# Kernel optimization log

Hardware: AMD Instinct MI355X
Metric: run time of the kernel (lower is better)

Reference implementation:

```python
import jax, jax.numpy as jnp
import numpy as np

# Reconstructed GTS forecasting module (DCGRU encoder-decoder, eval mode / no teacher forcing).
N = 5000        # nodes_num
U = 32          # rnn_units
IN = 1          # node_features per step
K = 2           # max_diffusion_step -> supports [X, A@X, A@A@X]
T_ENC = 12
T_DEC = 12
DIN = (K + 1) * (IN + U)


def setup_inputs() -> dict:
    key = jax.random.key(0)
    ks = jax.random.split(key, 12)
    def p(k, shape, scale=0.1):
        return jax.random.normal(k, shape, dtype=jnp.float32) * scale
    inputs = jax.random.normal(ks[0], (N, T_ENC), dtype=jnp.float32)
    targets = jax.random.normal(ks[1], (N, T_DEC), dtype=jnp.float32)
    adj = jax.random.uniform(ks[2], (N, N), dtype=jnp.float32)
    adj = adj / jnp.sum(adj, axis=1, keepdims=True)  # random-walk normalized support
    return {
        'inputs': inputs, 'targets': targets, 'adj_matrix': adj,
        'enc_Wg': p(ks[3], (DIN, 2 * U)), 'enc_bg': jnp.zeros((2 * U,), jnp.float32),
        'enc_Wc': p(ks[4], (DIN, U)),     'enc_bc': jnp.zeros((U,), jnp.float32),
        'dec_Wg': p(ks[5], (DIN, 2 * U)), 'dec_bg': jnp.zeros((2 * U,), jnp.float32),
        'dec_Wc': p(ks[6], (DIN, U)),     'dec_bc': jnp.zeros((U,), jnp.float32),
        'dec_Wp': p(ks[7], (U, 1)),       'dec_bp': jnp.zeros((1,), jnp.float32),
    }


def _gconv(x, h, adj, W, b):
    # diffusion graph convolution over supports [I, A, A^2]
    xh = jnp.concatenate([x, h], axis=-1)          # [N, IN+U]
    x1 = adj @ xh                                  # [N, IN+U]
    x2 = adj @ x1                                  # [N, IN+U]
    return jnp.concatenate([xh, x1, x2], axis=-1) @ W + b


def _dcgru_step(x, h, adj, Wg, bg, Wc, bc):
    ru = jax.nn.sigmoid(_gconv(x, h, adj, Wg, bg))  # [N, 2U]
    r, u = jnp.split(ru, 2, axis=-1)
    c = jnp.tanh(_gconv(x, r * h, adj, Wc, bc))
    return u * h + (1.0 - u) * c


def reference(inputs, targets, adj_matrix, enc_Wg, enc_bg, enc_Wc, enc_bc,
              dec_Wg, dec_bg, dec_Wc, dec_bc, dec_Wp, dec_bp):
    # ---- encoder: scan DCGRU over encoder_length timesteps ----
    def enc_step(h, xt):  # xt: [N]
        h = _dcgru_step(xt[:, None], h, adj_matrix, enc_Wg, enc_bg, enc_Wc, enc_bc)
        return h, None
    h0 = jnp.zeros((N, U), inputs.dtype)
    h_enc, _ = jax.lax.scan(enc_step, h0, inputs.T)
    go = jnp.zeros((N, 1), inputs.dtype)
    def dec_step(carry, _):
        h, x = carry
        h = _dcgru_step(x, h, adj_matrix, dec_Wg, dec_bg, dec_Wc, dec_bc)
        out = h @ dec_Wp + dec_bp  # [N, 1]
        return (h, out), out
    _, outs = jax.lax.scan(dec_step, (h_enc, go), None, length=T_DEC)
    # torch.cat(outputs, dim=-1) -> [N, T_DEC]
    return outs[:, :, 0].T
```

## Files before the change

kernel.cpp:

```cpp
#include <hip/hip_runtime.h>
#include <type_traits>

constexpr int NN = 5000;
constexpr int NP = 5120;
constexpr int TT = 12;
constexpr int UU = 32;
constexpr int FP = 48;
constexpr int FR = 33;
constexpr int DN = 99;
constexpr int BN = 16;
constexpr int KC = 128;
constexpr int NKC = NP / KC;
constexpr int CPW = NKC / 8;
constexpr int GRID_MM = (NN + BN - 1) / BN;
constexpr int CHE = FP * KC;
constexpr int ACH = BN * KC;

typedef __attribute__((ext_vector_type(8))) short short8;
typedef __attribute__((ext_vector_type(4))) float f32x4;

__device__ __forceinline__ unsigned short f2bf(float x) {
  union { float f; unsigned u; } c; c.f = x;
  return (unsigned short)((c.u + 0x7FFFu + ((c.u >> 16) & 1u)) >> 16);
}

__device__ __forceinline__ int flatXF(int f, int node) {
  int chunk = node >> 7;
  int ks = (node >> 5) & 3;
  int q = (node >> 3) & 3;
  int j = node & 7;
  int t3 = f >> 4;
  int m = f & 15;
  return chunk * CHE + t3 * 2048 + ks * 512 + (m + 16 * q) * 8 + j;
}

__global__ void k_zero(uint4* __restrict__ p, int n) {
  int i = blockIdx.x * 256 + threadIdx.x;
  if (i < n) p[i] = make_uint4(0u, 0u, 0u, 0u);
}

__global__ void k_cast2(const float* __restrict__ adj, unsigned short* __restrict__ adjb) {
  int gid = blockIdx.x * 256 + threadIdx.x;
  int n = gid / (NP / 8);
  int kk = (gid % (NP / 8)) * 8;
  union { short8 s; unsigned short u[8]; } o;
  if (n < NN && kk < NN) {
    const f32x4* a = reinterpret_cast<const f32x4*>(adj + (size_t)n * NN + kk);
    f32x4 x0 = __builtin_nontemporal_load(a);
    f32x4 x1 = __builtin_nontemporal_load(a + 1);
    o.u[0] = f2bf(x0.x); o.u[1] = f2bf(x0.y); o.u[2] = f2bf(x0.z); o.u[3] = f2bf(x0.w);
    o.u[4] = f2bf(x1.x); o.u[5] = f2bf(x1.y); o.u[6] = f2bf(x1.z); o.u[7] = f2bf(x1.w);
  } else {
    o.u[0] = 0; o.u[1] = 0; o.u[2] = 0; o.u[3] = 0;
    o.u[4] = 0; o.u[5] = 0; o.u[6] = 0; o.u[7] = 0;
  }
  int nt = n >> 4, m = n & 15;
  int c = kk >> 7, ks = (kk >> 5) & 3, q = (kk >> 3) & 3;
  size_t d = ((size_t)(nt * NKC + c)) * ACH + ks * 512 + (q * 16 + m) * 8;
  *reinterpret_cast<short8*>(adjb + d) = o.s;
}

__global__ void k_initx0(const float* __restrict__ in, float* __restrict__ xf,
                         unsigned short* __restrict__ xb) {
  int n = blockIdx.x * 256 + threadIdx.x;
  if (n >= NP) return;
  float v = (n < NN) ? in[(size_t)n * TT] : 0.f;
  xf[n] = v;
  xb[flatXF(0, n)] = f2bf(v);
}

template <int EPI, bool USEBF>
__global__ __launch_bounds__(512, 4) void k_gemm(
    const unsigned short* __restrict__ adjb, const float* __restrict__ adjf,
    const unsigned short* __restrict__ rhs,
    float* __restrict__ outF, unsigned short* __restrict__ outB,
    const float* __restrict__ s0F, const float* __restrict__ s1F,
    const float* __restrict__ W, const float* __restrict__ bias,
    float* __restrict__ hT, float* __restrict__ uT,
    float* __restrict__ xoF, unsigned short* __restrict__ xoB,
    const float* __restrict__ inp, const float* __restrict__ Wp,
    const float* __restrict__ bp, float* __restrict__ dout,
    int mode, int tnext, int dstep) {
  constexpr int WC = (EPI == 1) ? 64 : 32;
  __shared__ float Pv[8 * FP * BN];
  __shared__ float x2s[(EPI > 0) ? FP * 17 : 1];
  __shared__ float Ws[(EPI > 0) ? DN * WC : 1];

  const int tid = threadIdx.x;
  const int wave = tid >> 6;
  const int lane = tid & 63;
  const int m = lane & 15;
  const int q = lane >> 4;
  const int nodeBase = blockIdx.x * BN;
  const int gn = nodeBase + m;
  const size_t ar = (size_t)((gn < NN) ? gn : NN - 1);

  f32x4 acc0 = {}, acc1 = {}, acc2 = {};
  short8 aCur[4], aNxt[4];

  auto loadA = [&](int i, short8* b) {
    if constexpr (USEBF) {
      const int ch = wave * CPW + i;
      const unsigned short* a0 =
          adjb + ((size_t)blockIdx.x * NKC + ch) * ACH + lane * 8;
#pragma unroll
      for (int ks = 0; ks < 4; ++ks)
        b[ks] = *reinterpret_cast<const short8*>(a0 + ks * 512);
    } else {
      const int k0 = (wave * CPW + i) * KC;
      const float* a0 = adjf + ar * NN;
#pragma unroll
      for (int ks = 0; ks < 4; ++ks) {
        int kb = k0 + ks * 32 + q * 8;
        union { short8 s; unsigned short u[8]; } p0;
        if (kb + 8 <= NN) {
          float4 x0 = *(const float4*)(a0 + kb);
          float4 x1 = *(const float4*)(a0 + kb + 4);
          p0.u[0] = f2bf(x0.x); p0.u[1] = f2bf(x0.y); p0.u[2] = f2bf(x0.z); p0.u[3] = f2bf(x0.w);
          p0.u[4] = f2bf(x1.x); p0.u[5] = f2bf(x1.y); p0.u[6] = f2bf(x1.z); p0.u[7] = f2bf(x1.w);
        } else {
          for (int j = 0; j < 8; ++j) {
            int k = kb + j;
            p0.u[j] = (k < NN) ? f2bf(a0[k]) : (unsigned short)0;
          }
        }
        b[ks] = p0.s;
      }
    }
  };

  loadA(0, aCur);
#pragma unroll
  for (int i = 0; i < CPW; ++i) {
    if (i + 1 < CPW) loadA(i + 1, aNxt);
    const int ch = wave * CPW + i;
    short8 cx[12];
    const unsigned short* xb = rhs + (size_t)ch * CHE + lane * 8;
#pragma unroll
    for (int t3 = 0; t3 < 3; ++t3)
#pragma unroll
      for (int ks = 0; ks < 4; ++ks)
        cx[t3 * 4 + ks] = *(const short8*)(xb + t3 * 2048 + ks * 512);
#pragma unroll
    for (int ks = 0; ks < 4; ++ks) {
      acc0 = __builtin_amdgcn_mfma_f32_16x16x32_bf16(cx[ks], aCur[ks], acc0, 0, 0, 0);
      acc1 = __builtin_amdgcn_mfma_f32_16x16x32_bf16(cx[4 + ks], aCur[ks], acc1, 0, 0, 0);
      acc2 = __builtin_amdgcn_mfma_f32_16x16x32_bf16(cx[8 + ks], aCur[ks], acc2, 0, 0, 0);
    }
#pragma unroll
    for (int ks = 0; ks < 4; ++ks) aCur[ks] = aNxt[ks];
  }

  if constexpr (EPI > 0) {
    for (int i = tid; i < DN * WC; i += 512) Ws[i] = W[i];
  }

#pragma unroll
  for (int r = 0; r < 4; ++r) {
    Pv[wave * (FP * BN) + (q * 4 + r) * BN + m] = acc0[r];
    Pv[wave * (FP * BN) + (16 + q * 4 + r) * BN + m] = acc1[r];
    Pv[wave * (FP * BN) + (32 + q * 4 + r) * BN + m] = acc2[r];
  }
  __syncthreads();

  if constexpr (EPI == 0) {
    for (int e = tid; e < FP * BN; e += 512) {
      int f = e >> 4, n = e & 15;
      float v = 0.f;
#pragma unroll
      for (int w = 0; w < 8; ++w) v += Pv[w * (FP * BN) + e];
      int gn2 = nodeBase + n;
      if (gn2 >= NN) v = 0.f;
      outF[(size_t)f * NP + gn2] = v;
      outB[flatXF(f, gn2)] = f2bf(v);
    }
  } else {
    for (int e = tid; e < FP * BN; e += 512) {
      int f = e >> 4, n = e & 15;
      float v = 0.f;
#pragma unroll
      for (int w = 0; w < 8; ++w) v += Pv[w * (FP * BN) + e];
      x2s[f * 17 + n] = v;
    }
    __syncthreads();
    const int nl = tid & 15;
    const int cg = tid >> 4;
    const int gn2 = nodeBase + nl;
    const bool valid = gn2 < NN;
    const int gnc = valid ? gn2 : NN - 1;
    if constexpr (EPI == 1) {
      float a0 = bias[cg], a1 = bias[cg + 32];
      for (int f = 0; f < FR; ++f) {
        float fe = s0F[(size_t)f * NP + gnc];
        a0 += fe * Ws[f * WC + cg]; a1 += fe * Ws[f * WC + cg + 32];
      }
      for (int f = 0; f < FR; ++f) {
        float fe = s1F[(size_t)f * NP + gnc];
        a0 += fe * Ws[(FR + f) * WC + cg]; a1 += fe * Ws[(FR + f) * WC + cg + 32];
      }
      for (int f = 0; f < FR; ++f) {
        float fe = x2s[f * 17 + nl];
        a0 += fe * Ws[(2 * FR + f) * WC + cg]; a1 += fe * Ws[(2 * FR + f) * WC + cg + 32];
      }
      float r = 1.f / (1.f + expf(-a0));
      float hv = hT[(size_t)cg * NP + gnc];
      float xc = valid ? r * hv : 0.f;
      xoF[(size_t)(1 + cg) * NP + gn2] = xc;
      xoB[flatXF(1 + cg, gn2)] = f2bf(xc);
      float u = 1.f / (1.f + expf(-a1));
      uT[(size_t)cg * NP + gn2] = valid ? u : 0.f;
      if (tid < BN) {
        int g3 = nodeBase + tid;
        float v0 = s0F[g3];
        xoF[g3] = v0;
        xoB[flatXF(0, g3)] = f2bf(v0);
      }
    } else {
      float a0 = bias[cg];
      for (int f = 0; f < FR; ++f) a0 += s0F[(size_t)f * NP + gnc] * Ws[f * WC + cg];
      for (int f = 0; f < FR; ++f) a0 += s1F[(size_t)f * NP + gnc] * Ws[(FR + f) * WC + cg];
      for (int f = 0; f < FR; ++f) a0 += x2s[f * 17 + nl] * Ws[(2 * FR + f) * WC + cg];
      float c = tanhf(a0);
      float u = uT[(size_t)cg * NP + gnc];
      float h0 = hT[(size_t)cg * NP + gnc];
      float hn = u * h0 + (1.f - u) * c;
      float hw = valid ? hn : 0.f;
      hT[(size_t)cg * NP + gn2] = hw;
      xoF[(size_t)(1 + cg) * NP + gn2] = hw;
      xoB[flatXF(1 + cg, gn2)] = f2bf(hw);
      __syncthreads();
      x2s[cg * 17 + nl] = hw;
      __syncthreads();
      if (tid < BN) {
        int g3 = nodeBase + tid;
        bool v3 = g3 < NN;
        float x0 = 0.f;
        if (mode == 0) {
          x0 = v3 ? inp[(size_t)g3 * TT + tnext] : 0.f;
        } else if (mode == 2) {
          float p = bp[0];
          for (int j = 0; j < UU; ++j) p += x2s[j * 17 + tid] * Wp[j];
          if (v3) dout[(size_t)g3 * TT + dstep] = p;
          x0 = v3 ? p : 0.f;
        }
        xoF[g3] = x0;
        xoB[flatXF(0, g3)] = f2bf(x0);
      }
    }
  }
}

extern "C" void kernel_launch(void* const* d_in, const int* in_sizes, int n_in,
                              void* d_out, int out_size, void* d_ws, size_t ws_size,
                              hipStream_t stream) {
  const float* inputs = (const float*)d_in[0];
  const float* adj = (const float*)d_in[2];
  const float* eWg = (const float*)d_in[3];
  const float* eBg = (const float*)d_in[4];
  const float* eWc = (const float*)d_in[5];
  const float* eBc = (const float*)d_in[6];
  const float* dWg = (const float*)d_in[7];
  const float* dBg = (const float*)d_in[8];
  const float* dWc = (const float*)d_in[9];
  const float* dBc = (const float*)d_in[10];
  const float* Wp = (const float*)d_in[11];
  const float* bp = (const float*)d_in[12];
  float* dout = (float*)d_out;

  char* ws = (char*)d_ws;
  size_t o = 0;
  float* xhGf = (float*)(ws + o); o += (size_t)FP * NP * 4;
  unsigned short* xhGb = (unsigned short*)(ws + o); o += (size_t)FP * NP * 2;
  float* xhCf = (float*)(ws + o); o += (size_t)FP * NP * 4;
  unsigned short* xhCb = (unsigned short*)(ws + o); o += (size_t)FP * NP * 2;
  float* x1f = (float*)(ws + o); o += (size_t)FP * NP * 4;
  unsigned short* x1b = (unsigned short*)(ws + o); o += (size_t)FP * NP * 2;
  float* hT = (float*)(ws + o); o += (size_t)UU * NP * 4;
  float* uT = (float*)(ws + o); o += (size_t)UU * NP * 4;
  size_t small = o;
  unsigned short* adjb = (unsigned short*)(ws + o);
  size_t need = o + (size_t)NP * NP * 2;
  bool usebf = ws_size >= need;

  k_zero<<<(int)((small / 16 + 255) / 256), 256, 0, stream>>>((uint4*)ws, (int)(small / 16));
  if (usebf) k_cast2<<<(NP / 8) * NP / 256, 256, 0, stream>>>(adj, adjb);
  k_initx0<<<NP / 256, 256, 0, stream>>>(inputs, xhGf, xhGb);

  auto run = [&](auto ubc) {
    constexpr bool UB = decltype(ubc)::value;
    const unsigned short* ab = UB ? adjb : nullptr;
    for (int t = 0; t < 2 * TT; ++t) {
      bool enc = t < TT;
      const float* Wg = enc ? eWg : dWg;
      const float* Bg = enc ? eBg : dBg;
      const float* Wc = enc ? eWc : dWc;
      const float* Bc = enc ? eBc : dBc;
      int mode, tn = 0, ds = 0;
      if (t < TT - 1) { mode = 0; tn = t + 1; }
      else if (t == TT - 1) { mode = 1; }
      else { mode = 2; ds = t - TT; }

      k_gemm<0, UB><<<GRID_MM, 512, 0, stream>>>(
          ab, adj, xhGb, x1f, x1b,
          nullptr, nullptr, nullptr, nullptr, nullptr, nullptr,
          nullptr, nullptr, nullptr, nullptr, nullptr, nullptr, 0, 0, 0);
      k_gemm<1, UB><<<GRID_MM, 512, 0, stream>>>(
          ab, adj, x1b, nullptr, nullptr,
          xhGf, x1f, Wg, Bg, hT, uT, xhCf, xhCb,
          nullptr, nullptr, nullptr, nullptr, 0, 0, 0);
      k_gemm<0, UB><<<GRID_MM, 512, 0, stream>>>(
          ab, adj, xhCb, x1f, x1b,
          nullptr, nullptr, nullptr, nullptr, nullptr, nullptr,
          nullptr, nullptr, nullptr, nullptr, nullptr, nullptr, 0, 0, 0);
      k_gemm<2, UB><<<GRID_MM, 512, 0, stream>>>(
          ab, adj, x1b, nullptr, nullptr,
          xhCf, x1f, Wc, Bc, hT, uT, xhGf, xhGb,
          inputs, Wp, bp, dout, mode, tn, ds);
    }
  };
  if (usebf) run(std::integral_constant<bool, true>{});
  else run(std::integral_constant<bool, false>{});
}
```

Before: 2.018 ms.

## Stream bf16 adjacency tiles into LDS with async global_load_lds pipeline

The bf16 GEMM path now issues direct global-to-LDS loads for the adjacency tiles four half-chunks ahead, using explicit vmcnt waits. The RHS fragments are double-buffered in registers at half-chunk granularity, which shrinks the register footprint and lets the MFMAs overlap with memory traffic. The cast kernel is reordered so that its writes to the tiled layout are contiguous. Shared memory becomes one 64KB aliased buffer, which may reduce occupancy, and the hand-coded waitcnt values must match the number of outstanding loads.

```diff
diff --git a/kernel.cpp b/kernel.cpp
--- a/kernel.cpp
+++ b/kernel.cpp
@@ -34,6 +34,19 @@
   return chunk * CHE + t3 * 2048 + ks * 512 + (m + 16 * q) * 8 + j;
 }
 
+template <int N>
+__device__ __forceinline__ void waitv() {
+  if constexpr (N == 0) asm volatile("s_waitcnt vmcnt(0)" ::: "memory");
+  else if constexpr (N == 6) asm volatile("s_waitcnt vmcnt(6)" ::: "memory");
+  else asm volatile("s_waitcnt vmcnt(8)" ::: "memory");
+}
+
+__device__ __forceinline__ void gl_lds16(const unsigned short* g, unsigned short* l) {
+  __builtin_amdgcn_global_load_lds(
+      (const __attribute__((address_space(1))) unsigned int*)g,
+      (__attribute__((address_space(3))) unsigned int*)l, 16, 0, 0);
+}
+
 __global__ void k_zero(uint4* __restrict__ p, int n) {
   int i = blockIdx.x * 256 + threadIdx.x;
   if (i < n) p[i] = make_uint4(0u, 0u, 0u, 0u);
@@ -41,11 +54,17 @@
 
 __global__ void k_cast2(const float* __restrict__ adj, unsigned short* __restrict__ adjb) {
   int gid = blockIdx.x * 256 + threadIdx.x;
-  int n = gid / (NP / 8);
-  int kk = (gid % (NP / 8)) * 8;
+  int tile = gid >> 8;
+  int r2 = gid & 255;
+  int nt = tile / NKC, c = tile - nt * NKC;
+  int ks = r2 >> 6;
+  int qm = r2 & 63;
+  int q = qm >> 4, m = qm & 15;
+  int n = nt * 16 + m;
+  int k = c * 128 + ks * 32 + q * 8;
   union { short8 s; unsigned short u[8]; } o;
-  if (n < NN && kk < NN) {
-    const f32x4* a = reinterpret_cast<const f32x4*>(adj + (size_t)n * NN + kk);
+  if (n < NN && k < NN) {
+    const f32x4* a = reinterpret_cast<const f32x4*>(adj + (size_t)n * NN + k);
     f32x4 x0 = __builtin_nontemporal_load(a);
     f32x4 x1 = __builtin_nontemporal_load(a + 1);
     o.u[0] = f2bf(x0.x); o.u[1] = f2bf(x0.y); o.u[2] = f2bf(x0.z); o.u[3] = f2bf(x0.w);
@@ -54,10 +73,7 @@
     o.u[0] = 0; o.u[1] = 0; o.u[2] = 0; o.u[3] = 0;
     o.u[4] = 0; o.u[5] = 0; o.u[6] = 0; o.u[7] = 0;
   }
-  int nt = n >> 4, m = n & 15;
-  int c = kk >> 7, ks = (kk >> 5) & 3, q = (kk >> 3) & 3;
-  size_t d = ((size_t)(nt * NKC + c)) * ACH + ks * 512 + (q * 16 + m) * 8;
-  *reinterpret_cast<short8*>(adjb + d) = o.s;
+  *reinterpret_cast<short8*>(adjb + (size_t)gid * 8) = o.s;
 }
 
 __global__ void k_initx0(const float* __restrict__ in, float* __restrict__ xf,
@@ -82,9 +98,11 @@
     const float* __restrict__ bp, float* __restrict__ dout,
     int mode, int tnext, int dstep) {
   constexpr int WC = (EPI == 1) ? 64 : 32;
-  __shared__ float Pv[8 * FP * BN];
-  __shared__ float x2s[(EPI > 0) ? FP * 17 : 1];
-  __shared__ float Ws[(EPI > 0) ? DN * WC : 1];
+  __shared__ __align__(16) char smem[65536];
+  float* Pv = (float*)smem;
+  float* Ws = (float*)(smem + 24576);
+  float* x2s = (float*)(smem + 49920);
+  unsigned short* ldsA = (unsigned short*)smem;
 
   const int tid = threadIdx.x;
   const int wave = tid >> 6;
@@ -93,20 +111,69 @@
   const int q = lane >> 4;
   const int nodeBase = blockIdx.x * BN;
   const int gn = nodeBase + m;
-  const size_t ar = (size_t)((gn < NN) ? gn : NN - 1);
 
   f32x4 acc0 = {}, acc1 = {}, acc2 = {};
-  short8 aCur[4], aNxt[4];
-
-  auto loadA = [&](int i, short8* b) {
-    if constexpr (USEBF) {
-      const int ch = wave * CPW + i;
-      const unsigned short* a0 =
-          adjb + ((size_t)blockIdx.x * NKC + ch) * ACH + lane * 8;
-#pragma unroll
-      for (int ks = 0; ks < 4; ++ks)
-        b[ks] = *reinterpret_cast<const short8*>(a0 + ks * 512);
-    } else {
+
+  if constexpr (USEBF) {
+    short8 cxA[6], cxB[6];
+
+#define CXBUF(JJ) ((((JJ) & 1) == 0) ? cxA : cxB)
+#define LOADCX(JJ, BUF)                                                        \
+  {                                                                            \
+    const unsigned short* xb_ =                                                \
+        rhs + (size_t)(wave * CPW + ((JJ) >> 1)) * CHE + ((JJ) & 1) * 1024 +   \
+        lane * 8;                                                              \
+    BUF[0] = *(const short8*)(xb_);                                            \
+    BUF[1] = *(const short8*)(xb_ + 512);                                      \
+    BUF[2] = *(const short8*)(xb_ + 2048);                                     \
+    BUF[3] = *(const short8*)(xb_ + 2560);                                     \
+    BUF[4] = *(const short8*)(xb_ + 4096);                                     \
+    BUF[5] = *(const short8*)(xb_ + 4608);                                     \
+  }
+#define STAGEA(JJ)                                                             \
+  {                                                                            \
+    const unsigned short* g_ =                                                 \
+        adjb +                                                                 \
+        ((size_t)blockIdx.x * NKC + wave * CPW + ((JJ) >> 1)) * ACH +          \
+        ((JJ) & 1) * 1024 + lane * 8;                                          \
+    unsigned short* l_ = ldsA + wave * 4096 + ((JJ) & 3) * 1024;               \
+    gl_lds16(g_, l_);                                                          \
+    gl_lds16(g_ + 512, l_ + 512);                                              \
+  }
+#define HITER(J)                                                               \
+  {                                                                            \
+    if constexpr ((J) + 1 < 10) LOADCX((J) + 1, CXBUF((J) + 1));               \
+    waitv<((J) <= 6) ? 8 : (((J) <= 8) ? 6 : 0)>();                            \
+    const short8* ap =                                                         \
+        (const short8*)(ldsA + wave * 4096 + ((J) & 3) * 1024 + lane * 8);     \
+    short8 ah0 = ap[0];                                                        \
+    short8 ah1 = ap[64];                                                       \
+    short8* cxc = CXBUF(J);                                                    \
+    acc0 = __builtin_amdgcn_mfma_f32_16x16x32_bf16(cxc[0], ah0, acc0, 0, 0, 0);\
+    acc1 = __builtin_amdgcn_mfma_f32_16x16x32_bf16(cxc[2], ah0, acc1, 0, 0, 0);\
+    acc2 = __builtin_amdgcn_mfma_f32_16x16x32_bf16(cxc[4], ah0, acc2, 0, 0, 0);\
+    acc0 = __builtin_amdgcn_mfma_f32_16x16x32_bf16(cxc[1], ah1, acc0, 0, 0, 0);\
+    acc1 = __builtin_amdgcn_mfma_f32_16x16x32_bf16(cxc[3], ah1, acc1, 0, 0, 0);\
+    acc2 = __builtin_amdgcn_mfma_f32_16x16x32_bf16(cxc[5], ah1, acc2, 0, 0, 0);\
+    __builtin_amdgcn_sched_barrier(0);                                         \
+    if constexpr ((J) + 4 < 10) STAGEA((J) + 4);                               \
+  }
+
+    STAGEA(0)
+    STAGEA(1)
+    STAGEA(2)
+    LOADCX(0, cxA)
+    STAGEA(3)
+    HITER(0) HITER(1) HITER(2) HITER(3) HITER(4)
+    HITER(5) HITER(6) HITER(7) HITER(8) HITER(9)
+#undef HITER
+#undef STAGEA
+#undef LOADCX
+#undef CXBUF
+  } else {
+    const size_t ar = (size_t)((gn < NN) ? gn : NN - 1);
+    short8 aCur[4], aNxt[4];
+    auto loadA = [&](int i, short8* b) {
       const int k0 = (wave * CPW + i) * KC;
       const float* a0 = adjf + ar * NN;
 #pragma unroll
@@ -126,30 +193,31 @@
         }
         b[ks] = p0.s;
       }
-    }
-  };
-
-  loadA(0, aCur);
-#pragma unroll
-  for (int i = 0; i < CPW; ++i) {
-    if (i + 1 < CPW) loadA(i + 1, aNxt);
-    const int ch = wave * CPW + i;
-    short8 cx[12];
-    const unsigned short* xb = rhs + (size_t)ch * CHE + lane * 8;
-#pragma unroll
-    for (int t3 = 0; t3 < 3; ++t3)
-#pragma unroll
-      for (int ks = 0; ks < 4; ++ks)
-        cx[t3 * 4 + ks] = *(const short8*)(xb + t3 * 2048 + ks * 512);
-#pragma unroll
-    for (int ks = 0; ks < 4; ++ks) {
-      acc0 = __builtin_amdgcn_mfma_f32_16x16x32_bf16(cx[ks], aCur[ks], acc0, 0, 0, 0);
-      acc1 = __builtin_amdgcn_mfma_f32_16x16x32_bf16(cx[4 + ks], aCur[ks], acc1, 0, 0, 0);
-      acc2 = __builtin_amdgcn_mfma_f32_16x16x32_bf16(cx[8 + ks], aCur[ks], acc2, 0, 0, 0);
-    }
-#pragma unroll
-    for (int ks = 0; ks < 4; ++ks) aCur[ks] = aNxt[ks];
-  }
+    };
+    loadA(0, aCur);
+#pragma unroll
+    for (int i = 0; i < CPW; ++i) {
+      if (i + 1 < CPW) loadA(i + 1, aNxt);
+      const int ch = wave * CPW + i;
+      short8 cx[12];
+      const unsigned short* xb = rhs + (size_t)ch * CHE + lane * 8;
+#pragma unroll
+      for (int t3 = 0; t3 < 3; ++t3)
+#pragma unroll
+        for (int ks = 0; ks < 4; ++ks)
+          cx[t3 * 4 + ks] = *(const short8*)(xb + t3 * 2048 + ks * 512);
+#pragma unroll
+      for (int ks = 0; ks < 4; ++ks) {
+        acc0 = __builtin_amdgcn_mfma_f32_16x16x32_bf16(cx[ks], aCur[ks], acc0, 0, 0, 0);
+        acc1 = __builtin_amdgcn_mfma_f32_16x16x32_bf16(cx[4 + ks], aCur[ks], acc1, 0, 0, 0);
+        acc2 = __builtin_amdgcn_mfma_f32_16x16x32_bf16(cx[8 + ks], aCur[ks], acc2, 0, 0, 0);
+      }
+#pragma unroll
+      for (int ks = 0; ks < 4; ++ks) aCur[ks] = aNxt[ks];
+    }
+  }
+
+  __syncthreads();
 
   if constexpr (EPI > 0) {
     for (int i = tid; i < DN * WC; i += 512) Ws[i] = W[i];
```

Result: slower. 2.789 ms (+38.2%).
